# Optimization experiments

Measured on AMD Instinct MI355X. Metric: run time of the kernel, lower is better.

## Reference

```python
import jax, jax.numpy as jnp
import numpy as np

B = 262144
D_MODEL = 128
T_STEPS = 100
BETA_START = 1e-4
BETA_END = 0.02


def setup_inputs() -> dict:
    key = jax.random.key(0)
    ks = jax.random.split(key, 6)
    s1 = 1.0 / np.sqrt(D_MODEL + 2)
    s2 = 1.0 / np.sqrt(D_MODEL)
    return {
        "context": jax.random.normal(ks[0], (B, D_MODEL), jnp.float32),
        "x_init": jax.random.normal(ks[1], (B, 1), jnp.float32),
        "noise": jax.random.normal(ks[2], (T_STEPS, B, 1), jnp.float32),
        "W1": jax.random.normal(ks[3], (D_MODEL + 2, D_MODEL), jnp.float32) * s1,
        "b1": jnp.zeros((D_MODEL,), jnp.float32),
        "W2": jax.random.normal(ks[4], (D_MODEL, D_MODEL), jnp.float32) * s2,
        "b2": jnp.zeros((D_MODEL,), jnp.float32),
        "W3": jax.random.normal(ks[5], (D_MODEL, 1), jnp.float32) * s2,
        "b3": jnp.zeros((1,), jnp.float32),
        "time_emb": jax.random.normal(jax.random.fold_in(key, 7), (T_STEPS, 1), jnp.float32) * 0.02,
    }


def reference(context, x_init, noise, W1, b1, W2, b2, W3, b3, time_emb):
    # Diffusion schedule (buffers in the torch module)
    betas = jnp.linspace(BETA_START, BETA_END, T_STEPS, dtype=jnp.float32)
    alphas = 1.0 - betas
    alphas_cumprod = jnp.cumprod(alphas)

    n = context.shape[0]

    def denoise(x, t_e):
        # concat [context (n,d), x (n,1), t_emb (n,1)] -> (n, d+2)
        inp = jnp.concatenate([context, x, jnp.broadcast_to(t_e, (n, 1))], axis=-1)
        h = jax.nn.silu(inp @ W1 + b1)
        h = jax.nn.silu(h @ W2 + b2)
        return h @ W3 + b3  # (n, 1)

    def step(x, scan_in):
        t, eps = scan_in  # t scalar int, eps (n,1)
        pred_noise = denoise(x, time_emb[t])
        alpha = alphas[t]
        acp = alphas_cumprod[t]
        beta = betas[t]
        eps_used = jnp.where(t > 0, 1.0, 0.0) * eps
        x_new = (x - beta / jnp.sqrt(1.0 - acp) * pred_noise) / jnp.sqrt(alpha) \
                + jnp.sqrt(beta) * eps_used
        return x_new, None

    ts = jnp.arange(T_STEPS - 1, -1, -1)  # reversed(range(T))
    x_final, _ = jax.lax.scan(step, x_init, (ts, noise))
    return x_final
```

## Files before the change

### kernel.cpp

```cpp
#include <hip/hip_runtime.h>

#define B_N 262144
#define T_STEPS 100
#define BETA_START 1e-4f
#define BETA_END 0.02f

typedef __bf16 bf16x8 __attribute__((ext_vector_type(8)));
typedef float f32x4 __attribute__((ext_vector_type(4)));

__device__ __forceinline__ float siluf(float z) {
  float e = __expf(-z);
  return z * __builtin_amdgcn_rcpf(1.0f + e);
}

__device__ __forceinline__ unsigned bbits(float f) {
  __bf16 h = (__bf16)f;
  return (unsigned)__builtin_bit_cast(unsigned short, h);
}
__device__ __forceinline__ unsigned pack2(float lo, float hi) {
  return bbits(lo) | (bbits(hi) << 16);
}
__device__ __forceinline__ float unlo(unsigned u) { return __uint_as_float(u << 16); }
__device__ __forceinline__ float unhi(unsigned u) { return __uint_as_float(u & 0xffff0000u); }

__global__ __launch_bounds__(256, 1) void diff_kernel(
    const float* __restrict__ ctx, const float* __restrict__ x_init,
    const float* __restrict__ noise, const float* __restrict__ W1,
    const float* __restrict__ b1, const float* __restrict__ W2,
    const float* __restrict__ b2, const float* __restrict__ W3,
    const float* __restrict__ b3, const float* __restrict__ temb,
    float* __restrict__ out) {
  __shared__ alignas(16) unsigned short sW[128][136];
  __shared__ float sx[128];
  __shared__ alignas(8) unsigned swxt[128];
  __shared__ float sb2[128];
  __shared__ float sw3[128];

  const int tid = threadIdx.x;
  const int lane = tid & 63;
  const int wv = tid >> 6;
  const int ar = lane & 15;
  const int kg = lane >> 4;
  const int rowW = blockIdx.x * 128 + wv * 32;

  for (int i = tid; i < 128 * 128; i += 256) {
    int k = i >> 7, n = i & 127;
    sW[n][k] = (unsigned short)bbits(W1[i]);
  }
  if (tid < 128) {
    swxt[tid] = pack2(W1[128 * 128 + tid], W1[129 * 128 + tid]);
    sb2[tid] = b2[tid];
    sw3[tid] = W3[tid];
  }
  __syncthreads();

  f32x4 acc[2][8];
#pragma unroll
  for (int nt = 0; nt < 8; ++nt) {
    float b1c = b1[nt * 16 + ar];
    acc[0][nt] = (f32x4){b1c, b1c, b1c, b1c};
    acc[1][nt] = acc[0][nt];
  }

  {
    bf16x8 caf[2][4];
#pragma unroll
    for (int t2 = 0; t2 < 2; ++t2) {
      const float* crow = ctx + (size_t)(rowW + t2 * 16 + ar) * 128;
#pragma unroll
      for (int kk = 0; kk < 4; ++kk)
#pragma unroll
        for (int j = 0; j < 8; ++j)
          caf[t2][kk][j] = (__bf16)crow[kk * 32 + kg * 8 + j];
    }
#pragma unroll
    for (int kk = 0; kk < 4; ++kk)
#pragma unroll
      for (int nt = 0; nt < 8; ++nt) {
        bf16x8 bf = *reinterpret_cast<const bf16x8*>(&sW[nt * 16 + ar][kk * 32 + kg * 8]);
        acc[0][nt] = __builtin_amdgcn_mfma_f32_16x16x32_bf16(caf[0][kk], bf, acc[0][nt], 0, 0, 0);
        acc[1][nt] = __builtin_amdgcn_mfma_f32_16x16x32_bf16(caf[1][kk], bf, acc[1][nt], 0, 0, 0);
      }
  }
  __syncthreads();

  unsigned c1p[2][4][4];
  {
    float* scr = reinterpret_cast<float*>(&sW[0][0]) + wv * 2112;
#pragma unroll
    for (int t2 = 0; t2 < 2; ++t2) {
#pragma unroll
      for (int nt = 0; nt < 8; ++nt)
#pragma unroll
        for (int r = 0; r < 4; ++r)
          scr[(kg * 4 + r) * 132 + nt * 16 + ar] = acc[t2][nt][r];
      asm volatile("s_waitcnt lgkmcnt(0)" ::: "memory");
#pragma unroll
      for (int kk = 0; kk < 4; ++kk)
#pragma unroll
        for (int jj = 0; jj < 4; ++jj) {
          float f0 = scr[ar * 132 + kk * 32 + kg * 8 + jj * 2];
          float f1 = scr[ar * 132 + kk * 32 + kg * 8 + jj * 2 + 1];
          c1p[t2][kk][jj] = pack2(f0, f1);
        }
      asm volatile("s_waitcnt lgkmcnt(0)" ::: "memory");
    }
  }
  __syncthreads();

  for (int i = tid; i < 128 * 128; i += 256) {
    int k = i >> 7, n = i & 127;
    sW[n][k] = (unsigned short)bbits(W2[i]);
  }

  float xq[2][4];
#pragma unroll
  for (int t2 = 0; t2 < 2; ++t2)
#pragma unroll
    for (int r = 0; r < 4; ++r)
      xq[t2][r] = x_init[rowW + t2 * 16 + kg * 4 + r];
  if (ar == 0) {
#pragma unroll
    for (int t2 = 0; t2 < 2; ++t2)
#pragma unroll
      for (int r = 0; r < 4; ++r)
        sx[wv * 32 + t2 * 16 + kg * 4 + r] = xq[t2][r];
  }

  const float db = (BETA_END - BETA_START) / 99.0f;
  float acp = 1.0f;
  for (int t = 0; t < T_STEPS; ++t) acp *= (1.0f - (BETA_START + (float)t * db));
  const float b3v = b3[0];
  __syncthreads();

  for (int t = T_STEPS - 1; t >= 0; --t) {
    const float beta = BETA_START + (float)t * db;
    const float alpha = 1.0f - beta;
    const float c_pred = beta * __builtin_amdgcn_rsqf(1.0f - acp);
    const float c_x = __builtin_amdgcn_rsqf(alpha);
    const float c_n = (t > 0) ? __builtin_amdgcn_sqrtf(beta) : 0.0f;
    const float te = temb[t];

    const size_t noff = (size_t)(T_STEPS - 1 - t) * B_N + rowW;
    const float eps0 = noise[noff + ar];
    const float eps1 = noise[noff + 16 + ar];
    const float xv0 = sx[wv * 32 + ar];
    const float xv1 = sx[wv * 32 + 16 + ar];

#pragma unroll
    for (int nt = 0; nt < 8; ++nt) {
      float b2v = sb2[nt * 16 + ar];
      acc[0][nt] = (f32x4){b2v, b2v, b2v, b2v};
      acc[1][nt] = acc[0][nt];
    }

#pragma unroll
    for (int kk = 0; kk < 4; ++kk) {
      bf16x8 af0, af1;
#pragma unroll
      for (int jj = 0; jj < 4; ++jj) {
        const unsigned cp0 = c1p[0][kk][jj], cp1 = c1p[1][kk][jj];
        const uint2 wp = *reinterpret_cast<const uint2*>(&swxt[kk * 32 + kg * 8 + 2 * jj]);
        const float wxe = unlo(wp.x), wxo = unlo(wp.y);
        const float ge = te * unhi(wp.x), go = te * unhi(wp.y);
        float z;
        z = fmaf(xv0, wxe, unlo(cp0) + ge); af0[2 * jj]     = (__bf16)siluf(z);
        z = fmaf(xv0, wxo, unhi(cp0) + go); af0[2 * jj + 1] = (__bf16)siluf(z);
        z = fmaf(xv1, wxe, unlo(cp1) + ge); af1[2 * jj]     = (__bf16)siluf(z);
        z = fmaf(xv1, wxo, unhi(cp1) + go); af1[2 * jj + 1] = (__bf16)siluf(z);
      }
#pragma unroll
      for (int nt = 0; nt < 8; ++nt) {
        bf16x8 bf = *reinterpret_cast<const bf16x8*>(&sW[nt * 16 + ar][kk * 32 + kg * 8]);
        acc[0][nt] = __builtin_amdgcn_mfma_f32_16x16x32_bf16(af0, bf, acc[0][nt], 0, 0, 0);
        acc[1][nt] = __builtin_amdgcn_mfma_f32_16x16x32_bf16(af1, bf, acc[1][nt], 0, 0, 0);
      }
    }

#pragma unroll
    for (int t2 = 0; t2 < 2; ++t2) {
      float p0 = 0.f, p1 = 0.f, p2 = 0.f, p3 = 0.f;
#pragma unroll
      for (int nt = 0; nt < 8; ++nt) {
        const float w3v = sw3[nt * 16 + ar];
        p0 = fmaf(siluf(acc[t2][nt][0]), w3v, p0);
        p1 = fmaf(siluf(acc[t2][nt][1]), w3v, p1);
        p2 = fmaf(siluf(acc[t2][nt][2]), w3v, p2);
        p3 = fmaf(siluf(acc[t2][nt][3]), w3v, p3);
      }
#pragma unroll
      for (int m = 1; m <= 8; m <<= 1) {
        p0 += __shfl_xor(p0, m, 64);
        p1 += __shfl_xor(p1, m, 64);
        p2 += __shfl_xor(p2, m, 64);
        p3 += __shfl_xor(p3, m, 64);
      }
      const float epsm = t2 ? eps1 : eps0;
      const float e0 = __shfl(epsm, kg * 4 + 0, 64);
      const float e1 = __shfl(epsm, kg * 4 + 1, 64);
      const float e2 = __shfl(epsm, kg * 4 + 2, 64);
      const float e3 = __shfl(epsm, kg * 4 + 3, 64);
      xq[t2][0] = fmaf(c_n, e0, (xq[t2][0] - c_pred * (p0 + b3v)) * c_x);
      xq[t2][1] = fmaf(c_n, e1, (xq[t2][1] - c_pred * (p1 + b3v)) * c_x);
      xq[t2][2] = fmaf(c_n, e2, (xq[t2][2] - c_pred * (p2 + b3v)) * c_x);
      xq[t2][3] = fmaf(c_n, e3, (xq[t2][3] - c_pred * (p3 + b3v)) * c_x);
      if (ar == 0) {
#pragma unroll
        for (int r = 0; r < 4; ++r)
          sx[wv * 32 + t2 * 16 + kg * 4 + r] = xq[t2][r];
      }
    }

    acp *= __builtin_amdgcn_rcpf(alpha);
  }

  if (ar == 0) {
#pragma unroll
    for (int t2 = 0; t2 < 2; ++t2)
#pragma unroll
      for (int r = 0; r < 4; ++r)
        out[rowW + t2 * 16 + kg * 4 + r] = xq[t2][r];
  }
}

extern "C" void kernel_launch(void* const* d_in, const int* in_sizes, int n_in,
                              void* d_out, int out_size, void* d_ws, size_t ws_size,
                              hipStream_t stream) {
  const float* ctx    = (const float*)d_in[0];
  const float* x_init = (const float*)d_in[1];
  const float* noise  = (const float*)d_in[2];
  const float* W1     = (const float*)d_in[3];
  const float* b1     = (const float*)d_in[4];
  const float* W2     = (const float*)d_in[5];
  const float* b2     = (const float*)d_in[6];
  const float* W3     = (const float*)d_in[7];
  const float* b3     = (const float*)d_in[8];
  const float* temb   = (const float*)d_in[9];
  float* out = (float*)d_out;

  diff_kernel<<<dim3(B_N / 128), dim3(256), 0, stream>>>(
      ctx, x_init, noise, W1, b1, W2, b2, W3, b3, temb, out);
}
```

Baseline: 2.843 ms.

## Halve rows per wave to cut registers and raise occupancy

Each wave now handles 16 rows instead of 32, so the block covers 64 rows and the grid doubles. Launch bounds move to 2 blocks per CU, and the accumulator and layer-1 cache register arrays are halved. The goal is more resident waves to hide MFMA, LDS and noise-load latency. The trade is that each sW B-fragment read from LDS now feeds only one MFMA instead of two, doubling LDS traffic per FLOP, and the per-block weight staging is repeated across twice as many blocks. Smaller changes ride along: context is loaded as float4, noise is read directly instead of via shuffles, and the z computation is written as fused FMAs.

```diff
diff --git a/kernel.cpp b/kernel.cpp
--- a/kernel.cpp
+++ b/kernel.cpp
@@ -23,7 +23,7 @@
 __device__ __forceinline__ float unlo(unsigned u) { return __uint_as_float(u << 16); }
 __device__ __forceinline__ float unhi(unsigned u) { return __uint_as_float(u & 0xffff0000u); }
 
-__global__ __launch_bounds__(256, 1) void diff_kernel(
+__global__ __launch_bounds__(256, 2) void diff_kernel(
     const float* __restrict__ ctx, const float* __restrict__ x_init,
     const float* __restrict__ noise, const float* __restrict__ W1,
     const float* __restrict__ b1, const float* __restrict__ W2,
@@ -31,7 +31,7 @@
     const float* __restrict__ b3, const float* __restrict__ temb,
     float* __restrict__ out) {
   __shared__ alignas(16) unsigned short sW[128][136];
-  __shared__ float sx[128];
+  __shared__ float sx[64];
   __shared__ alignas(8) unsigned swxt[128];
   __shared__ float sb2[128];
   __shared__ float sw3[128];
@@ -41,7 +41,7 @@
   const int wv = tid >> 6;
   const int ar = lane & 15;
   const int kg = lane >> 4;
-  const int rowW = blockIdx.x * 128 + wv * 32;
+  const int rowW = blockIdx.x * 64 + wv * 16;
 
   for (int i = tid; i < 128 * 128; i += 256) {
     int k = i >> 7, n = i & 127;
@@ -54,57 +54,52 @@
   }
   __syncthreads();
 
-  f32x4 acc[2][8];
+  f32x4 acc[8];
 #pragma unroll
   for (int nt = 0; nt < 8; ++nt) {
     float b1c = b1[nt * 16 + ar];
-    acc[0][nt] = (f32x4){b1c, b1c, b1c, b1c};
-    acc[1][nt] = acc[0][nt];
-  }
-
+    acc[nt] = (f32x4){b1c, b1c, b1c, b1c};
+  }
   {
-    bf16x8 caf[2][4];
-#pragma unroll
-    for (int t2 = 0; t2 < 2; ++t2) {
-      const float* crow = ctx + (size_t)(rowW + t2 * 16 + ar) * 128;
-#pragma unroll
-      for (int kk = 0; kk < 4; ++kk)
-#pragma unroll
-        for (int j = 0; j < 8; ++j)
-          caf[t2][kk][j] = (__bf16)crow[kk * 32 + kg * 8 + j];
+    const float4* crow4 = reinterpret_cast<const float4*>(ctx + (size_t)(rowW + ar) * 128);
+    bf16x8 caf[4];
+#pragma unroll
+    for (int kk = 0; kk < 4; ++kk) {
+      float4 a = crow4[kk * 8 + kg * 2];
+      float4 b = crow4[kk * 8 + kg * 2 + 1];
+      caf[kk][0] = (__bf16)a.x; caf[kk][1] = (__bf16)a.y;
+      caf[kk][2] = (__bf16)a.z; caf[kk][3] = (__bf16)a.w;
+      caf[kk][4] = (__bf16)b.x; caf[kk][5] = (__bf16)b.y;
+      caf[kk][6] = (__bf16)b.z; caf[kk][7] = (__bf16)b.w;
     }
 #pragma unroll
     for (int kk = 0; kk < 4; ++kk)
 #pragma unroll
       for (int nt = 0; nt < 8; ++nt) {
         bf16x8 bf = *reinterpret_cast<const bf16x8*>(&sW[nt * 16 + ar][kk * 32 + kg * 8]);
-        acc[0][nt] = __builtin_amdgcn_mfma_f32_16x16x32_bf16(caf[0][kk], bf, acc[0][nt], 0, 0, 0);
-        acc[1][nt] = __builtin_amdgcn_mfma_f32_16x16x32_bf16(caf[1][kk], bf, acc[1][nt], 0, 0, 0);
-      }
-  }
-  __syncthreads();
-
-  unsigned c1p[2][4][4];
+        acc[nt] = __builtin_amdgcn_mfma_f32_16x16x32_bf16(caf[kk], bf, acc[nt], 0, 0, 0);
+      }
+  }
+  __syncthreads();
+
+  unsigned c1p[4][4];
   {
     float* scr = reinterpret_cast<float*>(&sW[0][0]) + wv * 2112;
 #pragma unroll
-    for (int t2 = 0; t2 < 2; ++t2) {
-#pragma unroll
-      for (int nt = 0; nt < 8; ++nt)
-#pragma unroll
-        for (int r = 0; r < 4; ++r)
-          scr[(kg * 4 + r) * 132 + nt * 16 + ar] = acc[t2][nt][r];
-      asm volatile("s_waitcnt lgkmcnt(0)" ::: "memory");
-#pragma unroll
-      for (int kk = 0; kk < 4; ++kk)
-#pragma unroll
-        for (int jj = 0; jj < 4; ++jj) {
-          float f0 = scr[ar * 132 + kk * 32 + kg * 8 + jj * 2];
-          float f1 = scr[ar * 132 + kk * 32 + kg * 8 + jj * 2 + 1];
-          c1p[t2][kk][jj] = pack2(f0, f1);
-        }
-      asm volatile("s_waitcnt lgkmcnt(0)" ::: "memory");
-    }
+    for (int nt = 0; nt < 8; ++nt)
+#pragma unroll
+      for (int r = 0; r < 4; ++r)
+        scr[(kg * 4 + r) * 132 + nt * 16 + ar] = acc[nt][r];
+    asm volatile("s_waitcnt lgkmcnt(0)" ::: "memory");
+#pragma unroll
+    for (int kk = 0; kk < 4; ++kk)
+#pragma unroll
+      for (int jj = 0; jj < 4; ++jj) {
+        float f0 = scr[ar * 132 + kk * 32 + kg * 8 + jj * 2];
+        float f1 = scr[ar * 132 + kk * 32 + kg * 8 + jj * 2 + 1];
+        c1p[kk][jj] = pack2(f0, f1);
+      }
+    asm volatile("s_waitcnt lgkmcnt(0)" ::: "memory");
   }
   __syncthreads();
 
@@ -113,18 +108,12 @@
     sW[n][k] = (unsigned short)bbits(W2[i]);
   }
 
-  float xq[2][4];
-#pragma unroll
-  for (int t2 = 0; t2 < 2; ++t2)
-#pragma unroll
-    for (int r = 0; r < 4; ++r)
-      xq[t2][r] = x_init[rowW + t2 * 16 + kg * 4 + r];
+  float xq[4];
+#pragma unroll
+  for (int r = 0; r < 4; ++r) xq[r] = x_init[rowW + kg * 4 + r];
   if (ar == 0) {
 #pragma unroll
-    for (int t2 = 0; t2 < 2; ++t2)
-#pragma unroll
-      for (int r = 0; r < 4; ++r)
-        sx[wv * 32 + t2 * 16 + kg * 4 + r] = xq[t2][r];
+    for (int r = 0; r < 4; ++r) sx[wv * 16 + kg * 4 + r] = xq[r];
   }
 
   const float db = (BETA_END - BETA_START) / 99.0f;
@@ -141,74 +130,60 @@
     const float c_n = (t > 0) ? __builtin_amdgcn_sqrtf(beta) : 0.0f;
     const float te = temb[t];
 
-    const size_t noff = (size_t)(T_STEPS - 1 - t) * B_N + rowW;
-    const float eps0 = noise[noff + ar];
-    const float eps1 = noise[noff + 16 + ar];
-    const float xv0 = sx[wv * 32 + ar];
-    const float xv1 = sx[wv * 32 + 16 + ar];
+    const size_t noff = (size_t)(T_STEPS - 1 - t) * B_N + rowW + kg * 4;
+    float er[4];
+#pragma unroll
+    for (int r = 0; r < 4; ++r) er[r] = noise[noff + r];
+    const float xv = sx[wv * 16 + ar];
 
 #pragma unroll
     for (int nt = 0; nt < 8; ++nt) {
       float b2v = sb2[nt * 16 + ar];
-      acc[0][nt] = (f32x4){b2v, b2v, b2v, b2v};
-      acc[1][nt] = acc[0][nt];
+      acc[nt] = (f32x4){b2v, b2v, b2v, b2v};
     }
 
 #pragma unroll
     for (int kk = 0; kk < 4; ++kk) {
-      bf16x8 af0, af1;
+      bf16x8 af;
 #pragma unroll
       for (int jj = 0; jj < 4; ++jj) {
-        const unsigned cp0 = c1p[0][kk][jj], cp1 = c1p[1][kk][jj];
+        const unsigned cp = c1p[kk][jj];
         const uint2 wp = *reinterpret_cast<const uint2*>(&swxt[kk * 32 + kg * 8 + 2 * jj]);
-        const float wxe = unlo(wp.x), wxo = unlo(wp.y);
-        const float ge = te * unhi(wp.x), go = te * unhi(wp.y);
-        float z;
-        z = fmaf(xv0, wxe, unlo(cp0) + ge); af0[2 * jj]     = (__bf16)siluf(z);
-        z = fmaf(xv0, wxo, unhi(cp0) + go); af0[2 * jj + 1] = (__bf16)siluf(z);
-        z = fmaf(xv1, wxe, unlo(cp1) + ge); af1[2 * jj]     = (__bf16)siluf(z);
-        z = fmaf(xv1, wxo, unhi(cp1) + go); af1[2 * jj + 1] = (__bf16)siluf(z);
+        float z0 = fmaf(te, unhi(wp.x), fmaf(xv, unlo(wp.x), unlo(cp)));
+        float z1 = fmaf(te, unhi(wp.y), fmaf(xv, unlo(wp.y), unhi(cp)));
+        af[2 * jj]     = (__bf16)siluf(z0);
+        af[2 * jj + 1] = (__bf16)siluf(z1);
       }
 #pragma unroll
       for (int nt = 0; nt < 8; ++nt) {
         bf16x8 bf = *reinterpret_cast<const bf16x8*>(&sW[nt * 16 + ar][kk * 32 + kg * 8]);
-        acc[0][nt] = __builtin_amdgcn_mfma_f32_16x16x32_bf16(af0, bf, acc[0][nt], 0, 0, 0);
-        acc[1][nt] = __builtin_amdgcn_mfma_f32_16x16x32_bf16(af1, bf, acc[1][nt], 0, 0, 0);
-      }
-    }
-
-#pragma unroll
-    for (int t2 = 0; t2 < 2; ++t2) {
-      float p0 = 0.f, p1 = 0.f, p2 = 0.f, p3 = 0.f;
-#pragma unroll
-      for (int nt = 0; nt < 8; ++nt) {
-        const float w3v = sw3[nt * 16 + ar];
-        p0 = fmaf(siluf(acc[t2][nt][0]), w3v, p0);
-        p1 = fmaf(siluf(acc[t2][nt][1]), w3v, p1);
-        p2 = fmaf(siluf(acc[t2][nt][2]), w3v, p2);
-        p3 = fmaf(siluf(acc[t2][nt][3]), w3v, p3);
-      }
-#pragma unroll
-      for (int m = 1; m <= 8; m <<= 1) {
-        p0 += __shfl_xor(p0, m, 64);
-        p1 += __shfl_xor(p1, m, 64);
-        p2 += __shfl_xor(p2, m, 64);
-        p3 += __shfl_xor(p3, m, 64);
-      }
-      const float epsm = t2 ? eps1 : eps0;
-      const float e0 = __shfl(epsm, kg * 4 + 0, 64);
-      const float e1 = __shfl(epsm, kg * 4 + 1, 64);
-      const float e2 = __shfl(epsm, kg * 4 + 2, 64);
-      const float e3 = __shfl(epsm, kg * 4 + 3, 64);
-      xq[t2][0] = fmaf(c_n, e0, (xq[t2][0] - c_pred * (p0 + b3v)) * c_x);
-      xq[t2][1] = fmaf(c_n, e1, (xq[t2][1] - c_pred * (p1 + b3v)) * c_x);
-      xq[t2][2] = fmaf(c_n, e2, (xq[t2][2] - c_pred * (p2 + b3v)) * c_x);
-      xq[t2][3] = fmaf(c_n, e3, (xq[t2][3] - c_pred * (p3 + b3v)) * c_x);
-      if (ar == 0) {
-#pragma unroll
-        for (int r = 0; r < 4; ++r)
-          sx[wv * 32 + t2 * 16 + kg * 4 + r] = xq[t2][r];
-      }
+        acc[nt] = __builtin_amdgcn_mfma_f32_16x16x32_bf16(af, bf, acc[nt], 0, 0, 0);
+      }
+    }
+
+    float p0 = 0.f, p1 = 0.f, p2 = 0.f, p3 = 0.f;
+#pragma unroll
+    for (int nt = 0; nt < 8; ++nt) {
+      const float w3v = sw3[nt * 16 + ar];
+      p0 = fmaf(siluf(acc[nt][0]), w3v, p0);
+      p1 = fmaf(siluf(acc[nt][1]), w3v, p1);
+      p2 = fmaf(siluf(acc[nt][2]), w3v, p2);
+      p3 = fmaf(siluf(acc[nt][3]), w3v, p3);
+    }
+#pragma unroll
+    for (int m = 1; m <= 8; m <<= 1) {
+      p0 += __shfl_xor(p0, m, 64);
+      p1 += __shfl_xor(p1, m, 64);
+      p2 += __shfl_xor(p2, m, 64);
+      p3 += __shfl_xor(p3, m, 64);
+    }
+    xq[0] = fmaf(c_n, er[0], (xq[0] - c_pred * (p0 + b3v)) * c_x);
+    xq[1] = fmaf(c_n, er[1], (xq[1] - c_pred * (p1 + b3v)) * c_x);
+    xq[2] = fmaf(c_n, er[2], (xq[2] - c_pred * (p2 + b3v)) * c_x);
+    xq[3] = fmaf(c_n, er[3], (xq[3] - c_pred * (p3 + b3v)) * c_x);
+    if (ar == 0) {
+#pragma unroll
+      for (int r = 0; r < 4; ++r) sx[wv * 16 + kg * 4 + r] = xq[r];
     }
 
     acp *= __builtin_amdgcn_rcpf(alpha);
@@ -216,10 +191,7 @@
 
   if (ar == 0) {
 #pragma unroll
-    for (int t2 = 0; t2 < 2; ++t2)
-#pragma unroll
-      for (int r = 0; r < 4; ++r)
-        out[rowW + t2 * 16 + kg * 4 + r] = xq[t2][r];
+    for (int r = 0; r < 4; ++r) out[rowW + kg * 4 + r] = xq[r];
   }
 }
 
@@ -238,6 +210,6 @@
   const float* temb   = (const float*)d_in[9];
   float* out = (float*)d_out;
 
-  diff_kernel<<<dim3(B_N / 128), dim3(256), 0, stream>>>(
+  diff_kernel<<<dim3(B_N / 64), dim3(256), 0, stream>>>(
       ctx, x_init, noise, W1, b1, W2, b2, W3, b3, temb, out);
 }
```

Measured after the change: 8.080 ms. 184% more time.

## Fold -log2e into weights, switch to fp16 MFMA, DPP row reductions, 2 blocks/CU

Applied to the files above, without the earlier changes.

Pre-scales W1, b1, b2 by -log2(e) and W3 by -ln2 so SiLU becomes a single exp2 plus reciprocal, with no negation or multiply inside the loop. Switches the MFMA operands and packed layer-1 values from bf16 to fp16, packed with cvt_pkrtz. Hoists the per-column weights and biases into registers instead of LDS, replaces shuffle reductions with DPP row rotations, and has only lane 0 of each row read the noise. Launch bounds now ask for 2 blocks per CU to improve latency hiding, which adds register pressure, and fp16 narrows the dynamic range compared with bf16.

```diff
diff --git a/kernel.cpp b/kernel.cpp
--- a/kernel.cpp
+++ b/kernel.cpp
@@ -4,26 +4,42 @@
 #define T_STEPS 100
 #define BETA_START 1e-4f
 #define BETA_END 0.02f
-
-typedef __bf16 bf16x8 __attribute__((ext_vector_type(8)));
+#define NLOG2E (-1.44269504088896340736f)
+#define NLN2 (-0.69314718055994530942f)
+
+typedef _Float16 f16x8 __attribute__((ext_vector_type(8)));
+typedef _Float16 f16x2 __attribute__((ext_vector_type(2)));
 typedef float f32x4 __attribute__((ext_vector_type(4)));
-
-__device__ __forceinline__ float siluf(float z) {
-  float e = __expf(-z);
-  return z * __builtin_amdgcn_rcpf(1.0f + e);
-}
-
-__device__ __forceinline__ unsigned bbits(float f) {
-  __bf16 h = (__bf16)f;
-  return (unsigned)__builtin_bit_cast(unsigned short, h);
-}
-__device__ __forceinline__ unsigned pack2(float lo, float hi) {
-  return bbits(lo) | (bbits(hi) << 16);
-}
-__device__ __forceinline__ float unlo(unsigned u) { return __uint_as_float(u << 16); }
-__device__ __forceinline__ float unhi(unsigned u) { return __uint_as_float(u & 0xffff0000u); }
-
-__global__ __launch_bounds__(256, 1) void diff_kernel(
+typedef unsigned u32x4 __attribute__((ext_vector_type(4)));
+
+__device__ __forceinline__ unsigned short f16b(float f) {
+  return __builtin_bit_cast(unsigned short, (_Float16)f);
+}
+
+__device__ __forceinline__ unsigned pkrtz(float a, float b) {
+  return __builtin_bit_cast(unsigned, __builtin_amdgcn_cvt_pkrtz(a, b));
+}
+
+__device__ __forceinline__ float sscale(float zs) {
+  float e = __builtin_amdgcn_exp2f(zs);
+  return zs * __builtin_amdgcn_rcpf(1.0f + e);
+}
+
+template <int CTRL>
+__device__ __forceinline__ float rrot_add(float x) {
+  int xi = __builtin_bit_cast(int, x);
+  int yi = __builtin_amdgcn_update_dpp(xi, xi, CTRL, 0xf, 0xf, false);
+  return x + __builtin_bit_cast(float, yi);
+}
+__device__ __forceinline__ float rowsum16(float x) {
+  x = rrot_add<0x128>(x);
+  x = rrot_add<0x124>(x);
+  x = rrot_add<0x122>(x);
+  x = rrot_add<0x121>(x);
+  return x;
+}
+
+__global__ __launch_bounds__(256, 2) void diff_kernel(
     const float* __restrict__ ctx, const float* __restrict__ x_init,
     const float* __restrict__ noise, const float* __restrict__ W1,
     const float* __restrict__ b1, const float* __restrict__ W2,
@@ -32,9 +48,6 @@
     float* __restrict__ out) {
   __shared__ alignas(16) unsigned short sW[128][136];
   __shared__ float sx[128];
-  __shared__ alignas(8) unsigned swxt[128];
-  __shared__ float sb2[128];
-  __shared__ float sw3[128];
 
   const int tid = threadIdx.x;
   const int lane = tid & 63;
@@ -45,41 +58,40 @@
 
   for (int i = tid; i < 128 * 128; i += 256) {
     int k = i >> 7, n = i & 127;
-    sW[n][k] = (unsigned short)bbits(W1[i]);
-  }
-  if (tid < 128) {
-    swxt[tid] = pack2(W1[128 * 128 + tid], W1[129 * 128 + tid]);
-    sb2[tid] = b2[tid];
-    sw3[tid] = W3[tid];
+    sW[n][k] = f16b(NLOG2E * W1[i]);
   }
   __syncthreads();
 
   f32x4 acc[2][8];
 #pragma unroll
   for (int nt = 0; nt < 8; ++nt) {
-    float b1c = b1[nt * 16 + ar];
-    acc[0][nt] = (f32x4){b1c, b1c, b1c, b1c};
+    float v = NLOG2E * b1[nt * 16 + ar];
+    acc[0][nt] = (f32x4){v, v, v, v};
     acc[1][nt] = acc[0][nt];
   }
-
   {
-    bf16x8 caf[2][4];
+    f16x8 caf[2][4];
 #pragma unroll
     for (int t2 = 0; t2 < 2; ++t2) {
-      const float* crow = ctx + (size_t)(rowW + t2 * 16 + ar) * 128;
-#pragma unroll
-      for (int kk = 0; kk < 4; ++kk)
-#pragma unroll
-        for (int j = 0; j < 8; ++j)
-          caf[t2][kk][j] = (__bf16)crow[kk * 32 + kg * 8 + j];
+      const float4* crow4 =
+          reinterpret_cast<const float4*>(ctx + (size_t)(rowW + t2 * 16 + ar) * 128);
+#pragma unroll
+      for (int kk = 0; kk < 4; ++kk) {
+        float4 a = crow4[kk * 8 + kg * 2];
+        float4 b = crow4[kk * 8 + kg * 2 + 1];
+        caf[t2][kk][0] = (_Float16)a.x; caf[t2][kk][1] = (_Float16)a.y;
+        caf[t2][kk][2] = (_Float16)a.z; caf[t2][kk][3] = (_Float16)a.w;
+        caf[t2][kk][4] = (_Float16)b.x; caf[t2][kk][5] = (_Float16)b.y;
+        caf[t2][kk][6] = (_Float16)b.z; caf[t2][kk][7] = (_Float16)b.w;
+      }
     }
 #pragma unroll
     for (int kk = 0; kk < 4; ++kk)
 #pragma unroll
       for (int nt = 0; nt < 8; ++nt) {
-        bf16x8 bf = *reinterpret_cast<const bf16x8*>(&sW[nt * 16 + ar][kk * 32 + kg * 8]);
-        acc[0][nt] = __builtin_amdgcn_mfma_f32_16x16x32_bf16(caf[0][kk], bf, acc[0][nt], 0, 0, 0);
-        acc[1][nt] = __builtin_amdgcn_mfma_f32_16x16x32_bf16(caf[1][kk], bf, acc[1][nt], 0, 0, 0);
+        f16x8 bf = *reinterpret_cast<const f16x8*>(&sW[nt * 16 + ar][kk * 32 + kg * 8]);
+        acc[0][nt] = __builtin_amdgcn_mfma_f32_16x16x32_f16(caf[0][kk], bf, acc[0][nt], 0, 0, 0);
+        acc[1][nt] = __builtin_amdgcn_mfma_f32_16x16x32_f16(caf[1][kk], bf, acc[1][nt], 0, 0, 0);
       }
   }
   __syncthreads();
@@ -101,7 +113,7 @@
         for (int jj = 0; jj < 4; ++jj) {
           float f0 = scr[ar * 132 + kk * 32 + kg * 8 + jj * 2];
           float f1 = scr[ar * 132 + kk * 32 + kg * 8 + jj * 2 + 1];
-          c1p[t2][kk][jj] = pack2(f0, f1);
+          c1p[t2][kk][jj] = pkrtz(f0, f1);
         }
       asm volatile("s_waitcnt lgkmcnt(0)" ::: "memory");
     }
@@ -110,7 +122,23 @@
 
   for (int i = tid; i < 128 * 128; i += 256) {
     int k = i >> 7, n = i & 127;
-    sW[n][k] = (unsigned short)bbits(W2[i]);
+    sW[n][k] = f16b(W2[i]);
+  }
+
+  unsigned wx2[4][4], wt2[4][4];
+#pragma unroll
+  for (int kk = 0; kk < 4; ++kk)
+#pragma unroll
+    for (int jj = 0; jj < 4; ++jj) {
+      int c = kk * 32 + kg * 8 + 2 * jj;
+      wx2[kk][jj] = pkrtz(NLOG2E * W1[128 * 128 + c], NLOG2E * W1[128 * 128 + c + 1]);
+      wt2[kk][jj] = pkrtz(NLOG2E * W1[129 * 128 + c], NLOG2E * W1[129 * 128 + c + 1]);
+    }
+  float w3r[8], b2s[8];
+#pragma unroll
+  for (int nt = 0; nt < 8; ++nt) {
+    w3r[nt] = NLN2 * W3[nt * 16 + ar];
+    b2s[nt] = NLOG2E * b2[nt * 16 + ar];
   }
 
   float xq[2][4];
@@ -134,6 +162,9 @@
   __syncthreads();
 
   for (int t = T_STEPS - 1; t >= 0; --t) {
+    int off = 0;
+    asm volatile("" : "+v"(off));
+
     const float beta = BETA_START + (float)t * db;
     const float alpha = 1.0f - beta;
     const float c_pred = beta * __builtin_amdgcn_rsqf(1.0f - acp);
@@ -141,70 +172,66 @@
     const float c_n = (t > 0) ? __builtin_amdgcn_sqrtf(beta) : 0.0f;
     const float te = temb[t];
 
-    const size_t noff = (size_t)(T_STEPS - 1 - t) * B_N + rowW;
-    const float eps0 = noise[noff + ar];
-    const float eps1 = noise[noff + 16 + ar];
     const float xv0 = sx[wv * 32 + ar];
     const float xv1 = sx[wv * 32 + 16 + ar];
 
 #pragma unroll
     for (int nt = 0; nt < 8; ++nt) {
-      float b2v = sb2[nt * 16 + ar];
-      acc[0][nt] = (f32x4){b2v, b2v, b2v, b2v};
+      acc[0][nt] = (f32x4){b2s[nt], b2s[nt], b2s[nt], b2s[nt]};
       acc[1][nt] = acc[0][nt];
     }
 
 #pragma unroll
     for (int kk = 0; kk < 4; ++kk) {
-      bf16x8 af0, af1;
-#pragma unroll
-      for (int jj = 0; jj < 4; ++jj) {
-        const unsigned cp0 = c1p[0][kk][jj], cp1 = c1p[1][kk][jj];
-        const uint2 wp = *reinterpret_cast<const uint2*>(&swxt[kk * 32 + kg * 8 + 2 * jj]);
-        const float wxe = unlo(wp.x), wxo = unlo(wp.y);
-        const float ge = te * unhi(wp.x), go = te * unhi(wp.y);
-        float z;
-        z = fmaf(xv0, wxe, unlo(cp0) + ge); af0[2 * jj]     = (__bf16)siluf(z);
-        z = fmaf(xv0, wxo, unhi(cp0) + go); af0[2 * jj + 1] = (__bf16)siluf(z);
-        z = fmaf(xv1, wxe, unlo(cp1) + ge); af1[2 * jj]     = (__bf16)siluf(z);
-        z = fmaf(xv1, wxo, unhi(cp1) + go); af1[2 * jj + 1] = (__bf16)siluf(z);
+      f16x8 af0, af1;
+      {
+        u32x4 a0, a1;
+#pragma unroll
+        for (int jj = 0; jj < 4; ++jj) {
+          f16x2 cp0 = __builtin_bit_cast(f16x2, c1p[0][kk][jj]);
+          f16x2 cp1 = __builtin_bit_cast(f16x2, c1p[1][kk][jj]);
+          f16x2 wx = __builtin_bit_cast(f16x2, wx2[kk][jj]);
+          f16x2 wt = __builtin_bit_cast(f16x2, wt2[kk][jj]);
+          float z00 = fmaf(te, (float)wt[0], fmaf(xv0, (float)wx[0], (float)cp0[0]));
+          float z01 = fmaf(te, (float)wt[1], fmaf(xv0, (float)wx[1], (float)cp0[1]));
+          float z10 = fmaf(te, (float)wt[0], fmaf(xv1, (float)wx[0], (float)cp1[0]));
+          float z11 = fmaf(te, (float)wt[1], fmaf(xv1, (float)wx[1], (float)cp1[1]));
+          a0[jj] = pkrtz(sscale(z00), sscale(z01));
+          a1[jj] = pkrtz(sscale(z10), sscale(z11));
+        }
+        af0 = __builtin_bit_cast(f16x8, a0);
+        af1 = __builtin_bit_cast(f16x8, a1);
       }
 #pragma unroll
       for (int nt = 0; nt < 8; ++nt) {
-        bf16x8 bf = *reinterpret_cast<const bf16x8*>(&sW[nt * 16 + ar][kk * 32 + kg * 8]);
-        acc[0][nt] = __builtin_amdgcn_mfma_f32_16x16x32_bf16(af0, bf, acc[0][nt], 0, 0, 0);
-        acc[1][nt] = __builtin_amdgcn_mfma_f32_16x16x32_bf16(af1, bf, acc[1][nt], 0, 0, 0);
-      }
-    }
-
+        f16x8 bf =
+            *reinterpret_cast<const f16x8*>(&sW[nt * 16 + ar][off + kk * 32 + kg * 8]);
+        acc[0][nt] = __builtin_amdgcn_mfma_f32_16x16x32_f16(af0, bf, acc[0][nt], 0, 0, 0);
+        acc[1][nt] = __builtin_amdgcn_mfma_f32_16x16x32_f16(af1, bf, acc[1][nt], 0, 0, 0);
+      }
+    }
+
+    const size_t nbase = (size_t)(T_STEPS - 1 - t) * B_N + rowW;
 #pragma unroll
     for (int t2 = 0; t2 < 2; ++t2) {
       float p0 = 0.f, p1 = 0.f, p2 = 0.f, p3 = 0.f;
 #pragma unroll
       for (int nt = 0; nt < 8; ++nt) {
-        const float w3v = sw3[nt * 16 + ar];
-        p0 = fmaf(siluf(acc[t2][nt][0]), w3v, p0);
-        p1 = fmaf(siluf(acc[t2][nt][1]), w3v, p1);
-        p2 = fmaf(siluf(acc[t2][nt][2]), w3v, p2);
-        p3 = fmaf(siluf(acc[t2][nt][3]), w3v, p3);
-      }
-#pragma unroll
-      for (int m = 1; m <= 8; m <<= 1) {
-        p0 += __shfl_xor(p0, m, 64);
-        p1 += __shfl_xor(p1, m, 64);
-        p2 += __shfl_xor(p2, m, 64);
-        p3 += __shfl_xor(p3, m, 64);
-      }
-      const float epsm = t2 ? eps1 : eps0;
-      const float e0 = __shfl(epsm, kg * 4 + 0, 64);
-      const float e1 = __shfl(epsm, kg * 4 + 1, 64);
-      const float e2 = __shfl(epsm, kg * 4 + 2, 64);
-      const float e3 = __shfl(epsm, kg * 4 + 3, 64);
-      xq[t2][0] = fmaf(c_n, e0, (xq[t2][0] - c_pred * (p0 + b3v)) * c_x);
-      xq[t2][1] = fmaf(c_n, e1, (xq[t2][1] - c_pred * (p1 + b3v)) * c_x);
-      xq[t2][2] = fmaf(c_n, e2, (xq[t2][2] - c_pred * (p2 + b3v)) * c_x);
-      xq[t2][3] = fmaf(c_n, e3, (xq[t2][3] - c_pred * (p3 + b3v)) * c_x);
+        p0 = fmaf(sscale(acc[t2][nt][0]), w3r[nt], p0);
+        p1 = fmaf(sscale(acc[t2][nt][1]), w3r[nt], p1);
+        p2 = fmaf(sscale(acc[t2][nt][2]), w3r[nt], p2);
+        p3 = fmaf(sscale(acc[t2][nt][3]), w3r[nt], p3);
+      }
+      p0 = rowsum16(p0);
+      p1 = rowsum16(p1);
+      p2 = rowsum16(p2);
+      p3 = rowsum16(p3);
       if (ar == 0) {
+        const float* np = noise + nbase + t2 * 16 + kg * 4;
+        xq[t2][0] = fmaf(c_n, np[0], (xq[t2][0] - c_pred * (p0 + b3v)) * c_x);
+        xq[t2][1] = fmaf(c_n, np[1], (xq[t2][1] - c_pred * (p1 + b3v)) * c_x);
+        xq[t2][2] = fmaf(c_n, np[2], (xq[t2][2] - c_pred * (p2 + b3v)) * c_x);
+        xq[t2][3] = fmaf(c_n, np[3], (xq[t2][3] - c_pred * (p3 + b3v)) * c_x);
 #pragma unroll
         for (int r = 0; r < 4; ++r)
           sx[wv * 32 + t2 * 16 + kg * 4 + r] = xq[t2][r];
```

After: 3.039 ms. 6.9% more time.
